# Kernel optimization log

Hardware: AMD Instinct MI355X
Metric: run time of the kernel (lower is better)

Reference implementation:

```python
import jax, jax.numpy as jnp
import numpy as np

H = 128  # hidden_dim
D = 128  # input_dim


def _lstm_scan(x_seq, Wih, Whh, bih, bhh, reverse=False):
    """x_seq: [T,B,Din]; returns h outputs [T,B,H] in original time order.
    PyTorch LSTMCell gate order: i, f, g, o."""
    hdim = Whh.shape[1]
    B = x_seq.shape[1]
    # Precompute input projections for all timesteps in one GEMM.
    xg = jnp.einsum('tbd,gd->tbg', x_seq, Wih) + bih  # [T,B,4H]

    def step(carry, xg_t):
        h, c = carry
        gates = xg_t + h @ Whh.T + bhh
        i, f, g, o = jnp.split(gates, 4, axis=-1)
        i = jax.nn.sigmoid(i)
        f = jax.nn.sigmoid(f)
        g = jnp.tanh(g)
        o = jax.nn.sigmoid(o)
        c = f * c + i * g
        h = o * jnp.tanh(c)
        return (h, c), h

    h0 = jnp.zeros((B, hdim), dtype=x_seq.dtype)
    c0 = jnp.zeros((B, hdim), dtype=x_seq.dtype)
    _, hs = jax.lax.scan(step, (h0, c0), xg, reverse=reverse)
    return hs  # [T,B,H], original time order (scan reverse handles bw dir)


def _bilstm_layer(x_seq, params_fw, params_bw):
    fw = _lstm_scan(x_seq, *params_fw, reverse=False)
    bw = _lstm_scan(x_seq, *params_bw, reverse=True)
    return jnp.concatenate([fw, bw], axis=-1)  # [T,B,2H]


def _make_cell_params(key, in_dim, hid):
    k1, k2, k3, k4 = jax.random.split(key, 4)
    s = 1.0 / np.sqrt(hid)
    return (
        jax.random.uniform(k1, (4 * hid, in_dim), jnp.float32, -s, s),
        jax.random.uniform(k2, (4 * hid, hid), jnp.float32, -s, s),
        jax.random.uniform(k3, (4 * hid,), jnp.float32, -s, s),
        jax.random.uniform(k4, (4 * hid,), jnp.float32, -s, s),
    )


def setup_inputs() -> dict:
    key = jax.random.key(0)
    ks = jax.random.split(key, 6)
    B, T = 64, 1024
    x = jax.random.normal(ks[0], (B, T, D), jnp.float32)
    lengths = jax.random.randint(ks[1], (B,), 1, T + 1, jnp.int64 if jax.config.jax_enable_x64 else jnp.int32)
    inp = {'x': x, 'lengths': lengths}
    names = ['fw1', 'bw1', 'fw2', 'bw2']
    in_dims = [D, D, 2 * H, 2 * H]
    for name, idim, k in zip(names, in_dims, ks[2:]):
        Wih, Whh, bih, bhh = _make_cell_params(k, idim, H)
        inp[f'Wih_{name}'] = Wih
        inp[f'Whh_{name}'] = Whh
        inp[f'bih_{name}'] = bih
        inp[f'bhh_{name}'] = bhh
    return inp


def reference(x, lengths,
              Wih_fw1, Whh_fw1, bih_fw1, bhh_fw1,
              Wih_bw1, Whh_bw1, bih_bw1, bhh_bw1,
              Wih_fw2, Whh_fw2, bih_fw2, bhh_fw2,
              Wih_bw2, Whh_bw2, bih_bw2, bhh_bw2):
    # lengths is unused in the original forward as well.
    xt = jnp.transpose(x, (1, 0, 2))  # [T,B,D] time-major for scan
    out1 = _bilstm_layer(xt,
                         (Wih_fw1, Whh_fw1, bih_fw1, bhh_fw1),
                         (Wih_bw1, Whh_bw1, bih_bw1, bhh_bw1))
    out2 = _bilstm_layer(out1,
                         (Wih_fw2, Whh_fw2, bih_fw2, bhh_fw2),
                         (Wih_bw2, Whh_bw2, bih_bw2, bhh_bw2))
    return jnp.transpose(out2, (1, 0, 2))  # [B,T,2H]
```

## Files before the change

kernel.cpp:

```cpp
#include <hip/hip_runtime.h>
#include <hip/hip_fp16.h>
#include <stdint.h>


#define T_SEQ 1024
#define B_SZ  64
#define M_TOT 65536

typedef _Float16 h2_t __attribute__((ext_vector_type(2)));
typedef _Float16 f16x8 __attribute__((ext_vector_type(8)));
typedef float f32x4 __attribute__((ext_vector_type(4)));

__device__ inline uint32_t pack2(float a, float b) {
  uint16_t ua = __builtin_bit_cast(uint16_t, (_Float16)a);
  uint16_t ub = __builtin_bit_cast(uint16_t, (_Float16)b);
  return (uint32_t)ua | ((uint32_t)ub << 16);
}

template <int CTRL>
__device__ inline float dppf(float v) {
  return __builtin_bit_cast(
      float, __builtin_amdgcn_update_dpp(0, __builtin_bit_cast(int, v), CTRL,
                                         0xF, 0xF, true));
}

__global__ void fused_prep(
    const float* __restrict__ Whh0, const float* __restrict__ Whh1,
    const float* __restrict__ Whh2, const float* __restrict__ Whh3,
    const float* __restrict__ Wih0, const float* __restrict__ Wih1,
    const float* __restrict__ Wih2, const float* __restrict__ Wih3,
    const float* __restrict__ bih0, const float* __restrict__ bih1,
    const float* __restrict__ bih2, const float* __restrict__ bih3,
    const float* __restrict__ bhh0, const float* __restrict__ bhh1,
    const float* __restrict__ bhh2, const float* __restrict__ bhh3,
    uint32_t* __restrict__ whbuf, uint32_t* __restrict__ btbuf1,
    uint32_t* __restrict__ btbuf2, float* __restrict__ biascat) {
  const int blk = blockIdx.x;
  const int tid = threadIdx.x;
  if (blk < 512) {
    int e = blk * 256 + tid;
    int c = e >> 15, e2 = e & 32767;
    const float* W = (c == 0) ? Whh0 : (c == 1) ? Whh1 : (c == 2) ? Whh2 : Whh3;
    int R = e2 >> 6, kw = e2 & 63;
    int g = ((R & 3) << 7) | (R >> 2);
    whbuf[c * 32768 + e2] = pack2(W[g * 128 + 2 * kw], W[g * 128 + 2 * kw + 1]);
  } else if (blk < 768) {
    int e = (blk - 512) * 256 + tid;
    int c = e >> 15, e2 = e & 32767;
    const float* W = c ? Wih1 : Wih0;
    int r = e2 >> 6, kw = e2 & 63;
    int g = ((r & 3) << 7) | (r >> 2);
    btbuf1[c * 32768 + e2] = pack2(W[g * 128 + 2 * kw], W[g * 128 + 2 * kw + 1]);
  } else if (blk < 1280) {
    int e = (blk - 768) * 256 + tid;
    int c = e >> 16, e2 = e & 65535;
    const float* W = c ? Wih3 : Wih2;
    int r = e2 >> 7, kw = e2 & 127;
    int g = ((r & 3) << 7) | (r >> 2);
    btbuf2[c * 65536 + e2] = pack2(W[g * 256 + 2 * kw], W[g * 256 + 2 * kw + 1]);
  } else {
    int e = (blk - 1280) * 256 + tid;
    int lc = e >> 9, gp = e & 511;
    const float* bi = (lc == 0) ? bih0 : (lc == 1) ? bih1 : (lc == 2) ? bih2 : bih3;
    const float* bh = (lc == 0) ? bhh0 : (lc == 1) ? bhh1 : (lc == 2) ? bhh2 : bhh3;
    int g = ((gp & 3) << 7) | (gp >> 2);
    biascat[e] = bi[g] + bh[g];
  }
}

__global__ void prep_x(const float2* __restrict__ x2, uint32_t* __restrict__ xf16) {
  int idx = blockIdx.x * 256 + threadIdx.x;
  float2 v = x2[idx];
  xf16[idx] = pack2(v.x, v.y);
}

template <int KW>
__global__ __launch_bounds__(256) void xg_gemm(
    const uint32_t* __restrict__ A, const uint32_t* __restrict__ Bt,
    const float* __restrict__ biascat, uint16_t* __restrict__ xg) {
  const int n0 = blockIdx.x * 64;
  const int m0 = blockIdx.y * 64;
  const int tid = threadIdx.x;
  __shared__ uint32_t At[64][36];
  __shared__ uint32_t Bts[64][36];
  const int lr = tid >> 2, lq = tid & 3;
  const int wave = tid >> 6, lane = tid & 63;
  const int wm = wave >> 1, wn = wave & 1;
  const int q = lane >> 4, ln16 = lane & 15;
  f32x4 acc[2][2] = {};
  for (int kb = 0; kb < KW; kb += 16) {
    uint4 av = *(const uint4*)&A[(size_t)(m0 + lr) * KW + kb + lq * 4];
    uint4 bv = *(const uint4*)&Bt[(size_t)(n0 + lr) * KW + kb + lq * 4];
    __syncthreads();
    *(uint4*)&At[lr][lq * 4] = av;
    *(uint4*)&Bts[lr][lq * 4] = bv;
    __syncthreads();
#pragma unroll
    for (int mi = 0; mi < 2; mi++) {
      f16x8 af = *(const f16x8*)&At[wm * 32 + mi * 16 + ln16][q * 4];
#pragma unroll
      for (int ni = 0; ni < 2; ni++) {
        f16x8 bf = *(const f16x8*)&Bts[wn * 32 + ni * 16 + ln16][q * 4];
        acc[mi][ni] = __builtin_amdgcn_mfma_f32_16x16x32_f16(af, bf, acc[mi][ni], 0, 0, 0);
      }
    }
  }
#pragma unroll
  for (int mi = 0; mi < 2; mi++)
#pragma unroll
    for (int ni = 0; ni < 2; ni++) {
      int n = n0 + wn * 32 + ni * 16 + ln16;
      int cell = n >> 9, gp = n & 511;
      float bs = biascat[n];
#pragma unroll
      for (int i = 0; i < 4; i++) {
        int m = m0 + wm * 32 + mi * 16 + q * 4 + i;
        float v = acc[mi][ni][i] + bs;
        xg[((size_t)cell * M_TOT + m) * 512 + gp] =
            __builtin_bit_cast(uint16_t, (_Float16)v);
      }
    }
}

template <bool FINAL>
__global__ __launch_bounds__(512, 2) void scan_kernel(
    const uint16_t* __restrict__ xg, const uint32_t* __restrict__ whB,
    uint16_t* __restrict__ hout, float* __restrict__ fout) {
  const int tid = threadIdx.x;
  const int j = tid >> 2;
  const int p = tid & 3;
  const int w = tid >> 6;
  const int lane = tid & 63;
  const int q = lane >> 4;
  const int ln16 = lane & 15;
  const int b = blockIdx.x & 63;
  const int dir = blockIdx.x >> 6;

  __shared__ __align__(16) uint32_t hbuf[2][64];

  f16x8 wb[4][4];
  {
    const uint32_t* wp = whB + (size_t)dir * 512 * 64;
#pragma unroll
    for (int nt = 0; nt < 4; nt++)
#pragma unroll
      for (int kt = 0; kt < 4; kt++)
        wb[nt][kt] = *(const f16x8*)&wp[(64 * w + 16 * nt + ln16) * 64 + 16 * kt + 4 * q];
  }
#pragma unroll
  for (int nt = 0; nt < 4; nt++)
#pragma unroll
    for (int kt = 0; kt < 4; kt++) asm volatile("" : "+v"(wb[nt][kt]));

  const float kmul = (p == 2) ? (-2.0f * 1.44269504f) : -1.44269504f;
  const float gm = (p == 2) ? 2.0f : 1.0f;
  const float gb = (p == 2) ? -1.0f : 0.0f;

  const uint16_t* xgp = xg + ((size_t)dir * M_TOT + (size_t)b * T_SEQ) * 512 + tid;

  if (tid < 64) hbuf[0][tid] = 0u;
  float c = 0.0f;
  const f32x4 zero4 = {0.0f, 0.0f, 0.0f, 0.0f};

  uint16_t xr[8];
#pragma unroll
  for (int k = 0; k < 4; k++) {
    const int tk = dir ? (T_SEQ - 1 - k) : k;
    xr[k] = xgp[(size_t)tk * 512];
  }
  __syncthreads();

  for (int s0 = 0; s0 < T_SEQ; s0 += 8) {
#pragma unroll
    for (int nt = 0; nt < 4; nt++)
#pragma unroll
      for (int kt = 0; kt < 4; kt++) asm volatile("" : "+v"(wb[nt][kt]));
#pragma unroll
    for (int k = 0; k < 8; k++) {
      const int s = s0 + k;
      const int par = k & 1;

      {
        const int tn = dir ? (T_SEQ - 1 - (s + 4)) : (s + 4);
        xr[(k + 4) & 7] = *(xgp + (ptrdiff_t)tn * 512);
      }

      const uint4* hb4 = (const uint4*)&hbuf[par][0];
      f32x4 a0, a1, a2, a3;
      {
        f16x8 hk = __builtin_bit_cast(f16x8, hb4[q]);
        a0 = __builtin_amdgcn_mfma_f32_16x16x32_f16(hk, wb[0][0], zero4, 0, 0, 0);
        a1 = __builtin_amdgcn_mfma_f32_16x16x32_f16(hk, wb[1][0], zero4, 0, 0, 0);
        a2 = __builtin_amdgcn_mfma_f32_16x16x32_f16(hk, wb[2][0], zero4, 0, 0, 0);
        a3 = __builtin_amdgcn_mfma_f32_16x16x32_f16(hk, wb[3][0], zero4, 0, 0, 0);
      }
#pragma unroll
      for (int kt = 1; kt < 4; kt++) {
        f16x8 hk = __builtin_bit_cast(f16x8, hb4[kt * 4 + q]);
        a0 = __builtin_amdgcn_mfma_f32_16x16x32_f16(hk, wb[0][kt], a0, 0, 0, 0);
        a1 = __builtin_amdgcn_mfma_f32_16x16x32_f16(hk, wb[1][kt], a1, 0, 0, 0);
        a2 = __builtin_amdgcn_mfma_f32_16x16x32_f16(hk, wb[2][kt], a2, 0, 0, 0);
        a3 = __builtin_amdgcn_mfma_f32_16x16x32_f16(hk, wb[3][kt], a3, 0, 0, 0);
      }
      float zs = (q & 2) ? ((q & 1) ? a3[0] : a2[0]) : ((q & 1) ? a1[0] : a0[0]);

      float z = zs + (float)__builtin_bit_cast(_Float16, xr[k]);

      float e = __builtin_amdgcn_exp2f(z * kmul);
      float sg = __builtin_amdgcn_rcpf(1.0f + e);
      float gv = __builtin_fmaf(sg, gm, gb);

      float gi = dppf<0x00>(gv);
      float gf = dppf<0x55>(gv);
      float gg = dppf<0xAA>(gv);
      float go = dppf<0xFF>(gv);

      c = __builtin_fmaf(gf, c, gi * gg);
      float ec = __builtin_amdgcn_exp2f(c * (-2.0f * 1.44269504f));
      float th = __builtin_fmaf(2.0f, __builtin_amdgcn_rcpf(1.0f + ec), -1.0f);
      float h = go * th;

      if (p == 0) {
        const int t = dir ? (T_SEQ - 1 - s) : s;
        uint16_t hu = __builtin_bit_cast(uint16_t, (_Float16)h);
        ((uint16_t*)(&hbuf[par ^ 1][0]))[j] = hu;
        if (FINAL) {
          fout[(size_t)(b * T_SEQ + t) * 256 + dir * 128 + j] = h;
        } else {
          hout[(size_t)(b * T_SEQ + t) * 256 + dir * 128 + j] = hu;
        }
      }
      asm volatile("s_waitcnt lgkmcnt(0)" ::: "memory");
      __builtin_amdgcn_s_barrier();
      asm volatile("" ::: "memory");
    }
  }
}

extern "C" void kernel_launch(void* const* d_in, const int* in_sizes, int n_in,
                              void* d_out, int out_size, void* d_ws, size_t ws_size,
                              hipStream_t stream) {
  const float* x = (const float*)d_in[0];
  const float* Wih_fw1 = (const float*)d_in[2];
  const float* Whh_fw1 = (const float*)d_in[3];
  const float* bih_fw1 = (const float*)d_in[4];
  const float* bhh_fw1 = (const float*)d_in[5];
  const float* Wih_bw1 = (const float*)d_in[6];
  const float* Whh_bw1 = (const float*)d_in[7];
  const float* bih_bw1 = (const float*)d_in[8];
  const float* bhh_bw1 = (const float*)d_in[9];
  const float* Wih_fw2 = (const float*)d_in[10];
  const float* Whh_fw2 = (const float*)d_in[11];
  const float* bih_fw2 = (const float*)d_in[12];
  const float* bhh_fw2 = (const float*)d_in[13];
  const float* Wih_bw2 = (const float*)d_in[14];
  const float* Whh_bw2 = (const float*)d_in[15];
  const float* bih_bw2 = (const float*)d_in[16];
  const float* bhh_bw2 = (const float*)d_in[17];

  uint8_t* ws = (uint8_t*)d_ws;
  uint32_t* whbuf = (uint32_t*)(ws + 0);
  uint32_t* btbuf1 = (uint32_t*)(ws + 524288);
  uint32_t* btbuf2 = (uint32_t*)(ws + 786432);
  float* biascat = (float*)(ws + 1310720);
  uint32_t* xf16 = (uint32_t*)(ws + 2097152);
  uint16_t* out1 = (uint16_t*)(ws + 18874368);
  uint16_t* xgbuf = (uint16_t*)(ws + 52428800);
  float* fout = (float*)d_out;

  fused_prep<<<1288, 256, 0, stream>>>(
      Whh_fw1, Whh_bw1, Whh_fw2, Whh_bw2,
      Wih_fw1, Wih_bw1, Wih_fw2, Wih_bw2,
      bih_fw1, bih_bw1, bih_fw2, bih_bw2,
      bhh_fw1, bhh_bw1, bhh_fw2, bhh_bw2,
      whbuf, btbuf1, btbuf2, biascat);
  prep_x<<<(B_SZ * T_SEQ * 64) / 256, 256, 0, stream>>>((const float2*)x, xf16);

  xg_gemm<64><<<dim3(16, 1024), 256, 0, stream>>>(xf16, btbuf1, biascat, xgbuf);
  scan_kernel<false><<<128, 512, 0, stream>>>(xgbuf, whbuf + 0, out1, nullptr);

  xg_gemm<128><<<dim3(16, 1024), 256, 0, stream>>>((const uint32_t*)out1, btbuf2,
                                                   biascat + 1024, xgbuf);
  scan_kernel<true><<<128, 512, 0, stream>>>(xgbuf, whbuf + 2 * 32768, nullptr, fout);
}
```

Measured before the change: 1.139 ms.

## Prefetch all K-chunks into registers and use 64-wide LDS tiles in xg GEMM

The input-projection GEMM now issues every global load for the whole K dimension into registers up front, then stages 64-column K chunks through a wider LDS tile. This replaces the old loop, which loaded 16 columns per iteration with two barriers each. The aim is fewer synchronisations and better latency hiding for global loads in this pre-scan GEMM. The cost is much higher register pressure, since KW=256 holds 32 uint4 values per thread, plus larger shared memory that may reduce occupancy.

```diff
diff --git a/kernel.cpp b/kernel.cpp
--- a/kernel.cpp
+++ b/kernel.cpp
@@ -81,42 +81,56 @@
   const int n0 = blockIdx.x * 64;
   const int m0 = blockIdx.y * 64;
   const int tid = threadIdx.x;
-  __shared__ uint32_t At[64][36];
-  __shared__ uint32_t Bts[64][36];
+  __shared__ uint32_t At[64][68];
+  __shared__ uint32_t Bts[64][68];
   const int lr = tid >> 2, lq = tid & 3;
   const int wave = tid >> 6, lane = tid & 63;
   const int wm = wave >> 1, wn = wave & 1;
   const int q = lane >> 4, ln16 = lane & 15;
+  constexpr int NCH = KW / 64;
+
+  uint4 avr[NCH][4], bvr[NCH][4];
+#pragma unroll
+  for (int ch = 0; ch < NCH; ch++)
+#pragma unroll
+    for (int i = 0; i < 4; i++) {
+      avr[ch][i] = *(const uint4*)&A[(size_t)(m0 + lr) * KW + ch * 64 + lq * 16 + 4 * i];
+      bvr[ch][i] = *(const uint4*)&Bt[(size_t)(n0 + lr) * KW + ch * 64 + lq * 16 + 4 * i];
+    }
+
   f32x4 acc[2][2] = {};
-  for (int kb = 0; kb < KW; kb += 16) {
-    uint4 av = *(const uint4*)&A[(size_t)(m0 + lr) * KW + kb + lq * 4];
-    uint4 bv = *(const uint4*)&Bt[(size_t)(n0 + lr) * KW + kb + lq * 4];
+#pragma unroll
+  for (int ch = 0; ch < NCH; ch++) {
+    if (ch) __syncthreads();
+#pragma unroll
+    for (int i = 0; i < 4; i++) {
+      *(uint4*)&At[lr][lq * 16 + 4 * i] = avr[ch][i];
+      *(uint4*)&Bts[lr][lq * 16 + 4 * i] = bvr[ch][i];
+    }
     __syncthreads();
-    *(uint4*)&At[lr][lq * 4] = av;
-    *(uint4*)&Bts[lr][lq * 4] = bv;
-    __syncthreads();
-#pragma unroll
-    for (int mi = 0; mi < 2; mi++) {
-      f16x8 af = *(const f16x8*)&At[wm * 32 + mi * 16 + ln16][q * 4];
-#pragma unroll
-      for (int ni = 0; ni < 2; ni++) {
-        f16x8 bf = *(const f16x8*)&Bts[wn * 32 + ni * 16 + ln16][q * 4];
-        acc[mi][ni] = __builtin_amdgcn_mfma_f32_16x16x32_f16(af, bf, acc[mi][ni], 0, 0, 0);
-      }
-    }
+#pragma unroll
+    for (int kt = 0; kt < 4; kt++)
+#pragma unroll
+      for (int mi = 0; mi < 2; mi++) {
+        f16x8 af = *(const f16x8*)&At[wm * 32 + mi * 16 + ln16][kt * 16 + q * 4];
+#pragma unroll
+        for (int ni = 0; ni < 2; ni++) {
+          f16x8 bf = *(const f16x8*)&Bts[wn * 32 + ni * 16 + ln16][kt * 16 + q * 4];
+          acc[mi][ni] = __builtin_amdgcn_mfma_f32_16x16x32_f16(af, bf, acc[mi][ni], 0, 0, 0);
+        }
+      }
   }
 #pragma unroll
   for (int mi = 0; mi < 2; mi++)
 #pragma unroll
     for (int ni = 0; ni < 2; ni++) {
       int n = n0 + wn * 32 + ni * 16 + ln16;
-      int cell = n >> 9, gp = n & 511;
       float bs = biascat[n];
 #pragma unroll
       for (int i = 0; i < 4; i++) {
         int m = m0 + wm * 32 + mi * 16 + q * 4 + i;
         float v = acc[mi][ni][i] + bs;
-        xg[((size_t)cell * M_TOT + m) * 512 + gp] =
+        xg[((size_t)(n >> 9) * M_TOT + m) * 512 + (n & 511)] =
             __builtin_bit_cast(uint16_t, (_Float16)v);
       }
     }
```

After: 1.402 ms. 1.23x slower.
